# Optimization experiments

Hardware: AMD Instinct MI355X
Metric: run time of the kernel (lower is better)

Reference implementation:

```python
import jax, jax.numpy as jnp
import numpy as np

D_MODEL = 1024
N_HEADS = 16
D_HEAD = D_MODEL // N_HEADS


def setup_inputs() -> dict:
    key = jax.random.key(0)
    ks = jax.random.split(key, 16)
    B, S, D = 2, 2048, D_MODEL
    s = 1.0 / np.sqrt(D)
    inp = {
        "query": jax.random.normal(ks[0], (B, S, D), jnp.float32),
        "key": jax.random.normal(ks[1], (B, S, D), jnp.float32),
        "value": jax.random.normal(ks[2], (B, S, D), jnp.float32),
        "pos_embedding": jax.random.normal(ks[3], (B, S, D), jnp.float32),
        "Wq": jax.random.normal(ks[4], (D, D), jnp.float32) * s,
        "bq": jnp.zeros((D,), jnp.float32),
        "Wk": jax.random.normal(ks[5], (D, D), jnp.float32) * s,
        "bk": jnp.zeros((D,), jnp.float32),
        "Wv": jax.random.normal(ks[6], (D, D), jnp.float32) * s,
        "bv": jnp.zeros((D,), jnp.float32),
        "Wpos": jax.random.normal(ks[7], (D, D), jnp.float32) * s,
        "u_bias": jax.random.normal(ks[8], (N_HEADS, D_HEAD), jnp.float32) * s,
        "v_bias": jax.random.normal(ks[9], (N_HEADS, D_HEAD), jnp.float32) * s,
        "Wout": jax.random.normal(ks[10], (D, D), jnp.float32) * s,
        "bout": jnp.zeros((D,), jnp.float32),
    }
    return inp


def _rel_shift(pos_score):
    # Transformer-XL relative shift: pad one zero column, reshape, drop first row.
    B, H, S1, S2 = pos_score.shape
    zeros = jnp.zeros((B, H, S1, 1), pos_score.dtype)
    padded = jnp.concatenate([zeros, pos_score], axis=-1)  # [B,H,S1,S2+1]
    padded = padded.reshape(B, H, S2 + 1, S1)
    return padded[:, :, 1:].reshape(B, H, S1, S2)


def reference(query, key, value, pos_embedding, Wq, bq, Wk, bk, Wv, bv, Wpos, u_bias, v_bias, Wout, bout):
    B, S, D = query.shape
    H, dh = N_HEADS, D_HEAD
    q = (query @ Wq + bq).reshape(B, S, H, dh)            # [B,S,H,dh]
    k = (key @ Wk + bk).reshape(B, S, H, dh)              # [B,S,H,dh]
    v = (value @ Wv + bv).reshape(B, S, H, dh)            # [B,S,H,dh]
    p = (pos_embedding @ Wpos).reshape(B, S, H, dh)       # [B,S,H,dh]

    content_score = jnp.einsum('bqhd,bkhd->bhqk', q + u_bias, k)
    pos_score = jnp.einsum('bqhd,bkhd->bhqk', q + v_bias, p)
    pos_score = _rel_shift(pos_score)

    score = (content_score + pos_score) / jnp.asarray(np.sqrt(D), score_dtype := content_score.dtype)
    attn = jax.nn.softmax(score, axis=-1)                 # [B,H,S,S]
    context = jnp.einsum('bhqk,bkhd->bqhd', attn, v).reshape(B, S, D)
    out = context @ Wout + bout
    return out, attn
```

## Files before the change

### kernel.cpp

```cpp
#include <hip/hip_runtime.h>

#define S_LEN 2048
#define DM    1024
#define NH    16
#define DH    64
#define BATCH 2
#define S2    ((size_t)S_LEN * S_LEN)

typedef _Float16 half_t;
typedef _Float16 f16x8 __attribute__((ext_vector_type(8)));
typedef _Float16 f16x4 __attribute__((ext_vector_type(4)));
typedef float    f32x4 __attribute__((ext_vector_type(4)));

__device__ __forceinline__ void gll16(const void* g, void* l) {
  __builtin_amdgcn_global_load_lds(
      (const __attribute__((address_space(1))) void*)g,
      (__attribute__((address_space(3))) void*)l, 16, 0, 0);
}

__device__ __forceinline__ void stage_gll(half_t* lds, const half_t* src, int stride) {
  const int t = threadIdx.x, w = t >> 6, lane = t & 63;
  const int c1 = lane & 7, r8 = lane >> 3;
#pragma unroll
  for (int it = 0; it < 4; ++it) {
    int r = w * 32 + it * 8 + r8;
    const half_t* g = src + (size_t)r * stride + ((c1 ^ r8) << 3);
    gll16(g, lds + (size_t)w * 2048 + it * 512);
  }
}

__device__ __forceinline__ void mfma_block(const half_t* At, const half_t* Bt,
                                           int w, int lane, f32x4 acc[2][8]) {
  const int grp = lane >> 4, li = lane & 15;
#pragma unroll
  for (int ks = 0; ks < 2; ++ks) {
    const int chunk = ks * 4 + grp;
    f16x8 a[2], b[8];
#pragma unroll
    for (int fr = 0; fr < 2; ++fr) {
      int r = w * 32 + fr * 16 + li;
      a[fr] = *(const f16x8*)&At[(size_t)(r * 8 + (chunk ^ (r & 7))) * 8];
    }
#pragma unroll
    for (int fc = 0; fc < 8; ++fc) {
      int r = fc * 16 + li;
      b[fc] = *(const f16x8*)&Bt[(size_t)(r * 8 + (chunk ^ (r & 7))) * 8];
    }
#pragma unroll
    for (int fr = 0; fr < 2; ++fr)
#pragma unroll
      for (int fc = 0; fc < 8; ++fc)
        acc[fr][fc] = __builtin_amdgcn_mfma_f32_16x16x32_f16(a[fr], b[fc], acc[fr][fc], 0, 0, 0);
  }
}

template<typename ST>
__device__ __forceinline__ void load8s(const ST* p, float* o) {
  if constexpr (sizeof(ST) == 2) {
    f16x8 v = *(const f16x8*)p;
#pragma unroll
    for (int e = 0; e < 8; ++e) o[e] = (float)v[e];
  } else {
    const float4* q = (const float4*)p;
    float4 a = q[0], b = q[1];
    o[0]=a.x; o[1]=a.y; o[2]=a.z; o[3]=a.w; o[4]=b.x; o[5]=b.y; o[6]=b.z; o[7]=b.w;
  }
}

struct PArgs {
  const float* asrc[4]; half_t* adst[4];
  const float* wsrc[5]; half_t* wdst[5];
};

__global__ __launch_bounds__(256) void prep(PArgs pa, half_t* zbuf) {
  __shared__ float T[64][65];
  const int bx = blockIdx.x, t = threadIdx.x;
  if (bx < 8192) {
    if (bx == 0 && t < 8) {
      float4 z = {0.f, 0.f, 0.f, 0.f};
      ((float4*)zbuf)[t] = z;
    }
    const int mat = bx >> 11, blk = bx & 2047;
    const float* s = pa.asrc[mat];
    half_t* d = pa.adst[mat];
    size_t i = ((size_t)blk * 256 + t) * 8;
    float4 v0 = *(const float4*)(s + i), v1 = *(const float4*)(s + i + 4);
    f16x8 h;
    h[0]=(half_t)v0.x; h[1]=(half_t)v0.y; h[2]=(half_t)v0.z; h[3]=(half_t)v0.w;
    h[4]=(half_t)v1.x; h[5]=(half_t)v1.y; h[6]=(half_t)v1.z; h[7]=(half_t)v1.w;
    *(f16x8*)(d + i) = h;
  } else {
    const int idx = bx - 8192;
    const int z = idx >> 8, rem = idx & 255;
    const int k0 = (rem & 15) * 64, n0 = (rem >> 4) * 64;
    const float* W = pa.wsrc[z];
    half_t* D = pa.wdst[z];
#pragma unroll
    for (int it = 0; it < 4; ++it) {
      int id2 = t + it * 256; int r = id2 >> 4, c4 = (id2 & 15) * 4;
      float4 v = *(const float4*)(W + (size_t)(k0 + r) * DM + n0 + c4);
      T[r][c4] = v.x; T[r][c4 + 1] = v.y; T[r][c4 + 2] = v.z; T[r][c4 + 3] = v.w;
    }
    __syncthreads();
#pragma unroll
    for (int it = 0; it < 2; ++it) {
      int id2 = t + it * 256; int n = id2 >> 3, kc = (id2 & 7) * 8;
      f16x8 o;
#pragma unroll
      for (int e = 0; e < 8; ++e) o[e] = (half_t)T[kc + e][n];
      *(f16x8*)&D[(size_t)(n0 + n) * DM + k0 + kc] = o;
    }
  }
}

struct GArgs {
  const half_t* A[4];  const half_t* Bt[4];
  const float* ba[4]; const float* bu[4]; const float* bv[4];
  half_t* oa[4]; half_t* ob[4]; float* of[4];
};

template<bool F32OUT>
__global__ __launch_bounds__(256) void gemm_k(GArgs g, int K) {
  __shared__ __align__(16) half_t At[128 * 64];
  __shared__ __align__(16) half_t Bt[128 * 64];
  const int z = blockIdx.z;
  const half_t* A = g.A[z];
  const half_t* B = g.Bt[z];
  const int n0 = blockIdx.x * 128, m0 = blockIdx.y * 128;
  const int t = threadIdx.x, w = t >> 6, lane = t & 63;
  const f32x4 zf = {0.f, 0.f, 0.f, 0.f};
  f32x4 acc[2][8];
#pragma unroll
  for (int i = 0; i < 2; ++i)
#pragma unroll
    for (int j = 0; j < 8; ++j) acc[i][j] = zf;

  for (int k0 = 0; k0 < K; k0 += 64) {
    stage_gll(At, A + (size_t)m0 * K + k0, K);
    stage_gll(Bt, B + (size_t)n0 * K + k0, K);
    __syncthreads();
    mfma_block(At, Bt, w, lane, acc);
    __syncthreads();
  }
  const int grp = lane >> 4, li = lane & 15;
#pragma unroll
  for (int fr = 0; fr < 2; ++fr)
#pragma unroll
    for (int fc = 0; fc < 8; ++fc)
#pragma unroll
      for (int r = 0; r < 4; ++r) {
        int row = m0 + w * 32 + fr * 16 + grp * 4 + r;
        int col = n0 + fc * 16 + li;
        float v = acc[fr][fc][r];
        if (g.ba[z]) v += g.ba[z][col];
        if constexpr (F32OUT) {
          g.of[z][(size_t)row * DM + col] = v;
        } else {
          float v1 = v + (g.bu[z] ? g.bu[z][col] : 0.f);
          g.oa[z][(size_t)row * DM + col] = (half_t)v1;
          if (g.ob[z]) g.ob[z][(size_t)row * DM + col] = (half_t)(v + g.bv[z][col]);
        }
      }
}

__global__ __launch_bounds__(256) void vtrans(const half_t* vp, half_t* vT) {
  __shared__ half_t T[64][72];
  const int s0 = blockIdx.x * 64, h = blockIdx.y, b = blockIdx.z;
  const int t = threadIdx.x;
#pragma unroll
  for (int it = 0; it < 2; ++it) {
    int idx = t + it * 256; int s = idx >> 3, c = idx & 7;
    uint4 v = *(const uint4*)(vp + ((size_t)(b * S_LEN + s0 + s)) * DM + h * DH + c * 8);
    *(uint4*)&T[s][c * 8] = v;
  }
  __syncthreads();
  half_t* dst = vT + ((size_t)(b * NH + h)) * DH * S_LEN;
#pragma unroll
  for (int it = 0; it < 2; ++it) {
    int idx = t + it * 256; int d = idx >> 3, sc = (idx & 7) * 8;
    f16x8 o;
#pragma unroll
    for (int e = 0; e < 8; ++e) o[e] = T[sc + e][d];
    *(f16x8*)&dst[(size_t)d * S_LEN + s0 + sc] = o;
  }
}

template<typename ST>
__global__ __launch_bounds__(512, 4) void score_fused(
    const half_t* __restrict__ qu_, const half_t* __restrict__ qv_,
    const half_t* __restrict__ kp_, const half_t* __restrict__ pp_,
    const half_t* __restrict__ zbuf, ST* __restrict__ sc, float* __restrict__ part)
{
  __shared__ __align__(16) half_t RegA[32768];
  __shared__ __align__(16) half_t QV[128 * 64];
  half_t* QU = RegA;
  half_t* Kt = RegA + 8192;
  half_t* Pb = RegA + 16384;
  half_t* Mf = RegA;

  const int bh = blockIdx.z, b = bh >> 4, h = bh & 15;
  const int kt = blockIdx.x, qt = blockIdx.y;
  const int i0 = qt * 128, k0 = kt * 128;
  const int base = 1920 + k0 - i0;
  const int t = threadIdx.x, w = t >> 6, lane = t & 63;
  const int grp = lane >> 4, li = lane & 15;

  {
    const half_t* srcA = qu_ + ((size_t)(b * S_LEN + i0)) * DM + h * DH;
    const half_t* srcB = kp_ + ((size_t)(b * S_LEN + k0)) * DM + h * DH;
    const half_t* srcQ = qv_ + ((size_t)(b * S_LEN + i0)) * DM + h * DH;
#pragma unroll
    for (int p = 0; p < 2; ++p) {
      int cidx = t + p * 512; int r = cidx >> 3, c = cidx & 7;
      size_t off = (size_t)r * DM + ((c ^ (r & 7)) << 3);
      gll16(srcA + off, QU + (size_t)cidx * 8);
      gll16(srcB + off, Kt + (size_t)cidx * 8);
      gll16(srcQ + off, QV + (size_t)cidx * 8);
    }
  }
#pragma unroll
  for (int p = 0; p < 4; ++p) {
    int cidx = t + p * 512; int e = cidx >> 3, c = cidx & 7;
    int jv = base + e; if (jv >= S_LEN + 1) jv -= (S_LEN + 1);
    const half_t* src = (jv == S_LEN)
        ? (zbuf + ((c ^ (e & 7)) << 3))
        : (pp_ + ((size_t)(b * S_LEN + jv)) * DM + h * DH + ((c ^ (e & 7)) << 3));
    gll16(src, Pb + (size_t)cidx * 8);
  }

  f16x8 aq[2];
  {
    int r128 = i0 + 128; if (r128 > S_LEN - 1) r128 = S_LEN - 1;
    const half_t* q128p = qv_ + ((size_t)(b * S_LEN + r128)) * DM + h * DH;
    aq[0] = *(const f16x8*)(q128p + (0 * 4 + grp) * 8);
    aq[1] = *(const f16x8*)(q128p + (1 * 4 + grp) * 8);
  }
  __syncthreads();

  const f32x4 zf = {0.f, 0.f, 0.f, 0.f};
  f32x4 acc_c[8];
#pragma unroll
  for (int j = 0; j < 8; ++j) acc_c[j] = zf;
#pragma unroll
  for (int kk = 0; kk < 2; ++kk) {
    const int chunk = kk * 4 + grp;
    int ra = w * 16 + li;
    f16x8 a = *(const f16x8*)&QU[(size_t)(ra * 8 + (chunk ^ (ra & 7))) * 8];
#pragma unroll
    for (int fc = 0; fc < 8; ++fc) {
      int rb = fc * 16 + li;
      f16x8 bf = *(const f16x8*)&Kt[(size_t)(rb * 8 + (chunk ^ (rb & 7))) * 8];
      acc_c[fc] = __builtin_amdgcn_mfma_f32_16x16x32_f16(a, bf, acc_c[fc], 0, 0, 0);
    }
  }
  f16x8 bm[2][2];
#pragma unroll
  for (int kk = 0; kk < 2; ++kk)
#pragma unroll
    for (int eci = 0; eci < 2; ++eci) {
      int rb = (w + eci * 8) * 16 + li;
      bm[kk][eci] = *(const f16x8*)&Pb[(size_t)(rb * 8 + ((kk * 4 + grp) ^ (rb & 7))) * 8];
    }
  __syncthreads();

  for (int rf = 0; rf < 8; ++rf) {
    f32x4 am[2] = {zf, zf};
#pragma unroll
    for (int kk = 0; kk < 2; ++kk) {
      int ra = rf * 16 + li;
      f16x8 a = *(const f16x8*)&QV[(size_t)(ra * 8 + ((kk * 4 + grp) ^ (ra & 7))) * 8];
#pragma unroll
      for (int eci = 0; eci < 2; ++eci)
        am[eci] = __builtin_amdgcn_mfma_f32_16x16x32_f16(a, bm[kk][eci], am[eci], 0, 0, 0);
    }
#pragma unroll
    for (int eci = 0; eci < 2; ++eci) {
      int ec = w + eci * 8;
      if (!(ec == 15 && li == 15)) {
        f16x4 hv;
#pragma unroll
        for (int r = 0; r < 4; ++r) hv[r] = (half_t)am[eci][r];
        *(f16x4*)&Mf[(size_t)(((ec * 8 + rf) * 4 + grp) * 64 + li * 4)] = hv;
      }
    }
  }

  {
    f32x4 am0 = zf;
#pragma unroll
    for (int kk = 0; kk < 2; ++kk)
      am0 = __builtin_amdgcn_mfma_f32_16x16x32_f16(aq[kk], bm[kk][0], am0, 0, 0, 0);
    if (grp == 0) {
      int e = w * 16 + li;
      Mf[(size_t)(((120 + (e >> 4)) * 4 + ((e >> 2) & 3)) * 64 + 60 + (e & 3))] = (half_t)am0[0];
    }
  }
  __syncthreads();

  ST* sb = sc + (size_t)bh * S2;
  float lsum[4] = {0.f, 0.f, 0.f, 0.f};
#pragma unroll
  for (int fc = 0; fc < 8; ++fc) {
#pragma unroll
    for (int rr = 0; rr < 4; ++rr) {
      int q = w * 16 + grp * 4 + rr;
      int k = fc * 16 + li;
      int e = k - q + 127;
      int jv = base + e;
      int dlt = (jv >= S_LEN + 1) ? 1 : 0;
      int rM = q + dlt;
      float mval;
      if (rM < 128) {
        int ec = e >> 4, ei = e & 15, rf = rM >> 4, ri = rM & 15;
        mval = (float)Mf[(size_t)(((ec * 8 + rf) * 4 + (ri >> 2)) * 64 + ei * 4 + (ri & 3))];
      } else {
        mval = (float)Mf[(size_t)(((120 + (e >> 4)) * 4 + ((e >> 2) & 3)) * 64 + 60 + (e & 3))];
      }
      float s = (acc_c[fc][rr] + mval) * 0.03125f;
      float ev = __expf(s);
      sb[(size_t)(i0 + q) * S_LEN + k0 + k] = (ST)ev;
      lsum[rr] += ev;
    }
  }
#pragma unroll
  for (int rr = 0; rr < 4; ++rr) {
    float v = lsum[rr];
#pragma unroll
    for (int d = 1; d < 16; d <<= 1) v += __shfl_xor(v, d);
    if (li == 0)
      part[((size_t)bh * S_LEN + i0 + w * 16 + grp * 4 + rr) * 16 + kt] = v;
  }
}

template<typename ST>
__global__ __launch_bounds__(256) void av_attn(const ST* sc, const half_t* vT, const float* part,
                                               float* attn, half_t* ctx) {
  __shared__ __align__(16) half_t Vt[2][64 * 128];
  __shared__ float Ls[128];
  const int bh = blockIdx.y, b = bh >> 4, h = bh & 15;
  const int q0 = blockIdx.x * 128;
  const int t = threadIdx.x;
  if (t < 128) {
    const float* pp = part + ((size_t)bh * S_LEN + q0 + t) * 16;
    float L = 0.f;
#pragma unroll
    for (int k = 0; k < 16; ++k) L += pp[k];
    Ls[t] = 1.f / L;
  }
  const ST* sb = sc + (size_t)bh * S2;
  float* ab = attn + (size_t)bh * S2;
  const half_t* vb = vT + (size_t)bh * (DH * S_LEN);
  const int w = t >> 6, lane = t & 63, grp = lane >> 4, li = lane & 15;
  const int c1 = lane & 15, d4 = lane >> 4;
  const f32x4 zf = {0.f, 0.f, 0.f, 0.f};
  f32x4 acc[2][4];
#pragma unroll
  for (int i = 0; i < 2; ++i)
#pragma unroll
    for (int j = 0; j < 4; ++j) acc[i][j] = zf;

#pragma unroll
  for (int it = 0; it < 4; ++it) {
    int d = w * 16 + it * 4 + d4;
    gll16(vb + (size_t)d * S_LEN + ((c1 ^ (d & 15)) << 3), Vt[0] + (size_t)w * 2048 + it * 512);
  }
  __syncthreads();
  int cur = 0;

  for (int kt = 0; kt < 16; ++kt) {
    if (kt + 1 < 16) {
#pragma unroll
      for (int it = 0; it < 4; ++it) {
        int d = w * 16 + it * 4 + d4;
        gll16(vb + (size_t)d * S_LEN + (kt + 1) * 128 + ((c1 ^ (d & 15)) << 3),
              Vt[cur ^ 1] + (size_t)w * 2048 + it * 512);
      }
    }
#pragma unroll
    for (int ks = 0; ks < 4; ++ks) {
      f16x8 pa[2];
#pragma unroll
      for (int fr = 0; fr < 2; ++fr) {
        int r128 = w * 32 + fr * 16 + li;
        int row = q0 + r128;
        int col = kt * 128 + ks * 32 + grp * 8;
        float sv[8];
        load8s(&sb[(size_t)row * S_LEN + col], sv);
        float rL = Ls[r128];
#pragma unroll
        for (int e = 0; e < 8; ++e) sv[e] *= rL;
        float4* dst = (float4*)&ab[(size_t)row * S_LEN + col];
        float4 w0 = {sv[0], sv[1], sv[2], sv[3]};
        float4 w1 = {sv[4], sv[5], sv[6], sv[7]};
        dst[0] = w0; dst[1] = w1;
        f16x8 ph;
#pragma unroll
        for (int e = 0; e < 8; ++e) ph[e] = (half_t)sv[e];
        pa[fr] = ph;
      }
      f16x8 bf[4];
#pragma unroll
      for (int fc = 0; fc < 4; ++fc) {
        int d = fc * 16 + li; int chunk = ks * 4 + grp;
        bf[fc] = *(const f16x8*)&Vt[cur][(size_t)(d * 16 + (chunk ^ (d & 15))) * 8];
      }
#pragma unroll
      for (int fr = 0; fr < 2; ++fr)
#pragma unroll
        for (int fc = 0; fc < 4; ++fc)
          acc[fr][fc] = __builtin_amdgcn_mfma_f32_16x16x32_f16(pa[fr], bf[fc], acc[fr][fc], 0, 0, 0);
    }
    __syncthreads();
    cur ^= 1;
  }
#pragma unroll
  for (int fr = 0; fr < 2; ++fr)
#pragma unroll
    for (int fc = 0; fc < 4; ++fc)
#pragma unroll
      for (int r = 0; r < 4; ++r) {
        int q = q0 + w * 32 + fr * 16 + grp * 4 + r;
        int d = fc * 16 + li;
        ctx[((size_t)(b * S_LEN + q)) * DM + h * DH + d] = (half_t)acc[fr][fc][r];
      }
}

extern "C" void kernel_launch(void* const* d_in, const int* in_sizes, int n_in,
                              void* d_out, int out_size, void* d_ws, size_t ws_size,
                              hipStream_t stream) {
  (void)in_sizes; (void)n_in; (void)out_size;

  const float* query  = (const float*)d_in[0];
  const float* key    = (const float*)d_in[1];
  const float* value  = (const float*)d_in[2];
  const float* pos    = (const float*)d_in[3];
  const float* Wq     = (const float*)d_in[4];
  const float* bq     = (const float*)d_in[5];
  const float* Wk     = (const float*)d_in[6];
  const float* bk     = (const float*)d_in[7];
  const float* Wv     = (const float*)d_in[8];
  const float* bv     = (const float*)d_in[9];
  const float* Wpos   = (const float*)d_in[10];
  const float* u_bias = (const float*)d_in[11];
  const float* v_bias = (const float*)d_in[12];
  const float* Wout   = (const float*)d_in[13];
  const float* bout   = (const float*)d_in[14];

  float* out  = (float*)d_out;
  float* attn = out + (size_t)BATCH * S_LEN * DM;

  char* ws = (char*)d_ws;
  half_t* Wt   = (half_t*)(ws);
  half_t* Af16 = (half_t*)(ws + 10485760);
  float*  part = (float*)(ws + 10485760);
  half_t* qu   = (half_t*)(ws + 44040192);
  half_t* qv   = (half_t*)(ws + 52428800);
  half_t* kp   = (half_t*)(ws + 60817408);
  half_t* pp   = (half_t*)(ws + 69206016);
  half_t* vp   = (half_t*)(ws + 77594624);
  half_t* vT   = (half_t*)(ws + 85983232);
  half_t* ctx  = (half_t*)(ws + 77594624);
  half_t* zbuf = (half_t*)(ws + 94371840);
  half_t* scH  = (half_t*)(ws + 94375936);
  const bool fast = ws_size >= (size_t)94375936 + (size_t)BATCH * NH * S2 * 2;

  dim3 blk(256);

  PArgs pa;
  pa.asrc[0] = query; pa.asrc[1] = key; pa.asrc[2] = value; pa.asrc[3] = pos;
  for (int i = 0; i < 4; ++i) pa.adst[i] = Af16 + (size_t)i * BATCH * S_LEN * DM;
  pa.wsrc[0] = Wq; pa.wsrc[1] = Wk; pa.wsrc[2] = Wv; pa.wsrc[3] = Wpos; pa.wsrc[4] = Wout;
  for (int i = 0; i < 5; ++i) pa.wdst[i] = Wt + (size_t)i * DM * DM;
  prep<<<dim3(8192 + 1280), blk, 0, stream>>>(pa, zbuf);

  GArgs ga{};
  for (int i = 0; i < 4; ++i) {
    ga.A[i]  = Af16 + (size_t)i * BATCH * S_LEN * DM;
    ga.Bt[i] = Wt + (size_t)i * DM * DM;
  }
  ga.ba[0] = bq; ga.ba[1] = bk; ga.ba[2] = bv; ga.ba[3] = nullptr;
  ga.bu[0] = u_bias; ga.bv[0] = v_bias;
  ga.oa[0] = qu; ga.oa[1] = kp; ga.oa[2] = vp; ga.oa[3] = pp;
  ga.ob[0] = qv;
  gemm_k<false><<<dim3(8, 32, 4), blk, 0, stream>>>(ga, DM);

  vtrans<<<dim3(32, 16, 2), blk, 0, stream>>>(vp, vT);

  dim3 g_sc(16, 16, 32);
  dim3 blk5(512);
  if (fast) {
    score_fused<half_t><<<g_sc, blk5, 0, stream>>>(qu, qv, kp, pp, zbuf, scH, part);
    av_attn<half_t><<<dim3(16, 32), blk, 0, stream>>>(scH, vT, part, attn, ctx);
  } else {
    float* scF = attn;
    score_fused<float><<<g_sc, blk5, 0, stream>>>(qu, qv, kp, pp, zbuf, scF, part);
    av_attn<float><<<dim3(16, 32), blk, 0, stream>>>(scF, vT, part, attn, ctx);
  }

  GArgs go{};
  go.A[0] = ctx; go.Bt[0] = Wt + (size_t)4 * DM * DM;
  go.ba[0] = bout; go.of[0] = out;
  gemm_k<true><<<dim3(8, 32, 1), blk, 0, stream>>>(go, DM);
}
```

Before: 548.7 us.

## Split AV attention over key dimension into two partial passes and combine

The attention-times-V kernel now runs over a third grid dimension that splits the 16 key tiles into two halves. Each half writes a partial fp16 context into its own workspace buffer, and a new combine2 kernel sums them into the final context. The original grid of 512 blocks was small relative to the GPU's CU count, so the split is meant to raise occupancy and parallelism. In exchange it adds an extra launch, extra context traffic, and an fp16 rounding of each partial sum before the add.

```diff
diff --git a/kernel.cpp b/kernel.cpp
--- a/kernel.cpp
+++ b/kernel.cpp
@@ -6,6 +6,7 @@
 #define DH    64
 #define BATCH 2
 #define S2    ((size_t)S_LEN * S_LEN)
+#define CTXSZ ((size_t)BATCH * S_LEN * DM)
 
 typedef _Float16 half_t;
 typedef _Float16 f16x8 __attribute__((ext_vector_type(8)));
@@ -334,11 +335,12 @@
 
 template<typename ST>
 __global__ __launch_bounds__(256) void av_attn(const ST* sc, const half_t* vT, const float* part,
-                                               float* attn, half_t* ctx) {
+                                               float* attn, half_t* ctxp) {
   __shared__ __align__(16) half_t Vt[2][64 * 128];
   __shared__ float Ls[128];
   const int bh = blockIdx.y, b = bh >> 4, h = bh & 15;
   const int q0 = blockIdx.x * 128;
+  const int kz = blockIdx.z;
   const int t = threadIdx.x;
   if (t < 128) {
     const float* pp = part + ((size_t)bh * S_LEN + q0 + t) * 16;
@@ -350,8 +352,10 @@
   const ST* sb = sc + (size_t)bh * S2;
   float* ab = attn + (size_t)bh * S2;
   const half_t* vb = vT + (size_t)bh * (DH * S_LEN);
+  half_t* ctx = ctxp + (size_t)kz * CTXSZ;
   const int w = t >> 6, lane = t & 63, grp = lane >> 4, li = lane & 15;
   const int c1 = lane & 15, d4 = lane >> 4;
+  const int kt0 = kz * 8, kt1 = kt0 + 8;
   const f32x4 zf = {0.f, 0.f, 0.f, 0.f};
   f32x4 acc[2][4];
 #pragma unroll
@@ -362,13 +366,14 @@
 #pragma unroll
   for (int it = 0; it < 4; ++it) {
     int d = w * 16 + it * 4 + d4;
-    gll16(vb + (size_t)d * S_LEN + ((c1 ^ (d & 15)) << 3), Vt[0] + (size_t)w * 2048 + it * 512);
+    gll16(vb + (size_t)d * S_LEN + kt0 * 128 + ((c1 ^ (d & 15)) << 3),
+          Vt[0] + (size_t)w * 2048 + it * 512);
   }
   __syncthreads();
   int cur = 0;
 
-  for (int kt = 0; kt < 16; ++kt) {
-    if (kt + 1 < 16) {
+  for (int kt = kt0; kt < kt1; ++kt) {
+    if (kt + 1 < kt1) {
 #pragma unroll
       for (int it = 0; it < 4; ++it) {
         int d = w * 16 + it * 4 + d4;
@@ -423,6 +428,16 @@
         int d = fc * 16 + li;
         ctx[((size_t)(b * S_LEN + q)) * DM + h * DH + d] = (half_t)acc[fr][fc][r];
       }
+}
+
+__global__ __launch_bounds__(256) void combine2(const half_t* a, const half_t* b, half_t* o) {
+  size_t i = ((size_t)blockIdx.x * 256 + threadIdx.x) * 8;
+  f16x8 va = *(const f16x8*)(a + i);
+  f16x8 vb = *(const f16x8*)(b + i);
+  f16x8 vo;
+#pragma unroll
+  for (int e = 0; e < 8; ++e) vo[e] = (half_t)((float)va[e] + (float)vb[e]);
+  *(f16x8*)(o + i) = vo;
 }
 
 extern "C" void kernel_launch(void* const* d_in, const int* in_sizes, int n_in,
@@ -453,6 +468,7 @@
   half_t* Wt   = (half_t*)(ws);
   half_t* Af16 = (half_t*)(ws + 10485760);
   float*  part = (float*)(ws + 10485760);
+  half_t* ctxp = (half_t*)(ws + 14680064);
   half_t* qu   = (half_t*)(ws + 44040192);
   half_t* qv   = (half_t*)(ws + 52428800);
   half_t* kp   = (half_t*)(ws + 60817408);
@@ -468,14 +484,14 @@
 
   PArgs pa;
   pa.asrc[0] = query; pa.asrc[1] = key; pa.asrc[2] = value; pa.asrc[3] = pos;
-  for (int i = 0; i < 4; ++i) pa.adst[i] = Af16 + (size_t)i * BATCH * S_LEN * DM;
+  for (int i = 0; i < 4; ++i) pa.adst[i] = Af16 + (size_t)i * CTXSZ;
   pa.wsrc[0] = Wq; pa.wsrc[1] = Wk; pa.wsrc[2] = Wv; pa.wsrc[3] = Wpos; pa.wsrc[4] = Wout;
   for (int i = 0; i < 5; ++i) pa.wdst[i] = Wt + (size_t)i * DM * DM;
   prep<<<dim3(8192 + 1280), blk, 0, stream>>>(pa, zbuf);
 
   GArgs ga{};
   for (int i = 0; i < 4; ++i) {
-    ga.A[i]  = Af16 + (size_t)i * BATCH * S_LEN * DM;
+    ga.A[i]  = Af16 + (size_t)i * CTXSZ;
     ga.Bt[i] = Wt + (size_t)i * DM * DM;
   }
   ga.ba[0] = bq; ga.ba[1] = bk; ga.ba[2] = bv; ga.ba[3] = nullptr;
@@ -490,12 +506,13 @@
   dim3 blk5(512);
   if (fast) {
     score_fused<half_t><<<g_sc, blk5, 0, stream>>>(qu, qv, kp, pp, zbuf, scH, part);
-    av_attn<half_t><<<dim3(16, 32), blk, 0, stream>>>(scH, vT, part, attn, ctx);
+    av_attn<half_t><<<dim3(16, 32, 2), blk, 0, stream>>>(scH, vT, part, attn, ctxp);
   } else {
     float* scF = attn;
     score_fused<float><<<g_sc, blk5, 0, stream>>>(qu, qv, kp, pp, zbuf, scF, part);
-    av_attn<float><<<dim3(16, 32), blk, 0, stream>>>(scF, vT, part, attn, ctx);
-  }
+    av_attn<float><<<dim3(16, 32, 2), blk, 0, stream>>>(scF, vT, part, attn, ctxp);
+  }
+  combine2<<<dim3((int)(CTXSZ / 8 / 256)), blk, 0, stream>>>(ctxp, ctxp + CTXSZ, ctx);
 
   GArgs go{};
   go.A[0] = ctx; go.Bt[0] = Wt + (size_t)4 * DM * DM;
```

Result: no change. 548.1 us (-0.1%).

## Shrink score kernel LDS by loading pos rows directly and storing shifted matrix

Applied to the files above, without the earlier changes.

The score kernel no longer stages the 256-row positional block in shared memory. Each thread loads its two positional B-fragments straight from global memory into registers. The positional scores are scattered during the MFMA epilogue into a pre-shifted 128x132 matrix, so the softmax loop reads them with a plain index instead of recomputing the relative shift. This cuts shared memory per block from about 80 KB to about 50 KB and raises the launch-bounds occupancy hint from 4 to 6. In exchange it adds uncoalesced global fragment loads and scattered 2-byte LDS stores that may hit bank conflicts.

```diff
diff --git a/kernel.cpp b/kernel.cpp
--- a/kernel.cpp
+++ b/kernel.cpp
@@ -6,10 +6,10 @@
 #define DH    64
 #define BATCH 2
 #define S2    ((size_t)S_LEN * S_LEN)
+#define CTXSZ ((size_t)BATCH * S_LEN * DM)
 
 typedef _Float16 half_t;
 typedef _Float16 f16x8 __attribute__((ext_vector_type(8)));
-typedef _Float16 f16x4 __attribute__((ext_vector_type(4)));
 typedef float    f32x4 __attribute__((ext_vector_type(4)));
 
 __device__ __forceinline__ void gll16(const void* g, void* l) {
@@ -186,17 +186,16 @@
 }
 
 template<typename ST>
-__global__ __launch_bounds__(512, 4) void score_fused(
+__global__ __launch_bounds__(512, 6) void score_fused(
     const half_t* __restrict__ qu_, const half_t* __restrict__ qv_,
     const half_t* __restrict__ kp_, const half_t* __restrict__ pp_,
     const half_t* __restrict__ zbuf, ST* __restrict__ sc, float* __restrict__ part)
 {
-  __shared__ __align__(16) half_t RegA[32768];
+  __shared__ __align__(16) half_t MsR[16896];
   __shared__ __align__(16) half_t QV[128 * 64];
-  half_t* QU = RegA;
-  half_t* Kt = RegA + 8192;
-  half_t* Pb = RegA + 16384;
-  half_t* Mf = RegA;
+  half_t* QU = MsR;
+  half_t* Kt = MsR + 8192;
+  half_t* Ms = MsR;
 
   const int bh = blockIdx.z, b = bh >> 4, h = bh & 15;
   const int kt = blockIdx.x, qt = blockIdx.y;
@@ -218,22 +217,20 @@
       gll16(srcQ + off, QV + (size_t)cidx * 8);
     }
   }
-#pragma unroll
-  for (int p = 0; p < 4; ++p) {
-    int cidx = t + p * 512; int e = cidx >> 3, c = cidx & 7;
-    int jv = base + e; if (jv >= S_LEN + 1) jv -= (S_LEN + 1);
-    const half_t* src = (jv == S_LEN)
-        ? (zbuf + ((c ^ (e & 7)) << 3))
-        : (pp_ + ((size_t)(b * S_LEN + jv)) * DM + h * DH + ((c ^ (e & 7)) << 3));
-    gll16(src, Pb + (size_t)cidx * 8);
-  }
-
-  f16x8 aq[2];
-  {
-    int r128 = i0 + 128; if (r128 > S_LEN - 1) r128 = S_LEN - 1;
-    const half_t* q128p = qv_ + ((size_t)(b * S_LEN + r128)) * DM + h * DH;
-    aq[0] = *(const f16x8*)(q128p + (0 * 4 + grp) * 8);
-    aq[1] = *(const f16x8*)(q128p + (1 * 4 + grp) * 8);
+
+  const int e0 = w * 16 + li, e1 = (w + 8) * 16 + li;
+  const int dlt0 = (base + e0 >= S_LEN + 1) ? 1 : 0;
+  const int dlt1 = (base + e1 >= S_LEN + 1) ? 1 : 0;
+  f16x8 bm[2][2];
+#pragma unroll
+  for (int eci = 0; eci < 2; ++eci) {
+    int e_row = eci ? e1 : e0;
+    int jv = base + e_row; if (jv >= S_LEN + 1) jv -= (S_LEN + 1);
+    const half_t* srcp = (jv == S_LEN) ? zbuf
+        : pp_ + ((size_t)(b * S_LEN + jv)) * DM + h * DH;
+#pragma unroll
+    for (int kk = 0; kk < 2; ++kk)
+      bm[kk][eci] = *(const f16x8*)(srcp + (kk * 4 + grp) * 8);
   }
   __syncthreads();
 
@@ -253,14 +250,6 @@
       acc_c[fc] = __builtin_amdgcn_mfma_f32_16x16x32_f16(a, bf, acc_c[fc], 0, 0, 0);
     }
   }
-  f16x8 bm[2][2];
-#pragma unroll
-  for (int kk = 0; kk < 2; ++kk)
-#pragma unroll
-    for (int eci = 0; eci < 2; ++eci) {
-      int rb = (w + eci * 8) * 16 + li;
-      bm[kk][eci] = *(const f16x8*)&Pb[(size_t)(rb * 8 + ((kk * 4 + grp) ^ (rb & 7))) * 8];
-    }
   __syncthreads();
 
   for (int rf = 0; rf < 8; ++rf) {
@@ -269,31 +258,37 @@
     for (int kk = 0; kk < 2; ++kk) {
       int ra = rf * 16 + li;
       f16x8 a = *(const f16x8*)&QV[(size_t)(ra * 8 + ((kk * 4 + grp) ^ (ra & 7))) * 8];
-#pragma unroll
-      for (int eci = 0; eci < 2; ++eci)
-        am[eci] = __builtin_amdgcn_mfma_f32_16x16x32_f16(a, bm[kk][eci], am[eci], 0, 0, 0);
+      am[0] = __builtin_amdgcn_mfma_f32_16x16x32_f16(a, bm[kk][0], am[0], 0, 0, 0);
+      am[1] = __builtin_amdgcn_mfma_f32_16x16x32_f16(a, bm[kk][1], am[1], 0, 0, 0);
     }
 #pragma unroll
     for (int eci = 0; eci < 2; ++eci) {
-      int ec = w + eci * 8;
-      if (!(ec == 15 && li == 15)) {
-        f16x4 hv;
-#pragma unroll
-        for (int r = 0; r < 4; ++r) hv[r] = (half_t)am[eci][r];
-        *(f16x4*)&Mf[(size_t)(((ec * 8 + rf) * 4 + grp) * 64 + li * 4)] = hv;
+      int e = eci ? e1 : e0;
+      int dlt = eci ? dlt1 : dlt0;
+#pragma unroll
+      for (int r = 0; r < 4; ++r) {
+        int rM = rf * 16 + grp * 4 + r;
+        int q = rM - dlt;
+        int k = e + q - 127;
+        if ((unsigned)q < 128u && (unsigned)k < 128u)
+          Ms[q * 132 + k] = (half_t)am[eci][r];
       }
     }
   }
 
   {
+    f16x8 aq0, aq1;
+    {
+      int r128 = i0 + 128; if (r128 > S_LEN - 1) r128 = S_LEN - 1;
+      const half_t* q128p = qv_ + ((size_t)(b * S_LEN + r128)) * DM + h * DH;
+      aq0 = *(const f16x8*)(q128p + (0 * 4 + grp) * 8);
+      aq1 = *(const f16x8*)(q128p + (1 * 4 + grp) * 8);
+    }
     f32x4 am0 = zf;
-#pragma unroll
-    for (int kk = 0; kk < 2; ++kk)
-      am0 = __builtin_amdgcn_mfma_f32_16x16x32_f16(aq[kk], bm[kk][0], am0, 0, 0, 0);
-    if (grp == 0) {
-      int e = w * 16 + li;
-      Mf[(size_t)(((120 + (e >> 4)) * 4 + ((e >> 2) & 3)) * 64 + 60 + (e & 3))] = (half_t)am0[0];
-    }
+    am0 = __builtin_amdgcn_mfma_f32_16x16x32_f16(aq0, bm[0][0], am0, 0, 0, 0);
+    am0 = __builtin_amdgcn_mfma_f32_16x16x32_f16(aq1, bm[1][0], am0, 0, 0, 0);
+    if (grp == 0 && dlt0 == 1)
+      Ms[127 * 132 + e0] = (half_t)am0[0];
   }
   __syncthreads();
 
@@ -305,17 +300,7 @@
     for (int rr = 0; rr < 4; ++rr) {
       int q = w * 16 + grp * 4 + rr;
       int k = fc * 16 + li;
-      int e = k - q + 127;
-      int jv = base + e;
-      int dlt = (jv >= S_LEN + 1) ? 1 : 0;
-      int rM = q + dlt;
-      float mval;
-      if (rM < 128) {
-        int ec = e >> 4, ei = e & 15, rf = rM >> 4, ri = rM & 15;
-        mval = (float)Mf[(size_t)(((ec * 8 + rf) * 4 + (ri >> 2)) * 64 + ei * 4 + (ri & 3))];
-      } else {
-        mval = (float)Mf[(size_t)(((120 + (e >> 4)) * 4 + ((e >> 2) & 3)) * 64 + 60 + (e & 3))];
-      }
+      float mval = (float)Ms[q * 132 + k];
       float s = (acc_c[fc][rr] + mval) * 0.03125f;
       float ev = __expf(s);
       sb[(size_t)(i0 + q) * S_LEN + k0 + k] = (ST)ev;
@@ -468,14 +453,14 @@
 
   PArgs pa;
   pa.asrc[0] = query; pa.asrc[1] = key; pa.asrc[2] = value; pa.asrc[3] = pos;
-  for (int i = 0; i < 4; ++i) pa.adst[i] = Af16 + (size_t)i * BATCH * S_LEN * DM;
+  for (int i = 0; i < 4; ++i) pa.adst[i] = Af16 + (size_t)i * CTXSZ;
   pa.wsrc[0] = Wq; pa.wsrc[1] = Wk; pa.wsrc[2] = Wv; pa.wsrc[3] = Wpos; pa.wsrc[4] = Wout;
   for (int i = 0; i < 5; ++i) pa.wdst[i] = Wt + (size_t)i * DM * DM;
   prep<<<dim3(8192 + 1280), blk, 0, stream>>>(pa, zbuf);
 
   GArgs ga{};
   for (int i = 0; i < 4; ++i) {
-    ga.A[i]  = Af16 + (size_t)i * BATCH * S_LEN * DM;
+    ga.A[i]  = Af16 + (size_t)i * CTXSZ;
     ga.Bt[i] = Wt + (size_t)i * DM * DM;
   }
   ga.ba[0] = bq; ga.ba[1] = bk; ga.ba[2] = bv; ga.ba[3] = nullptr;
```

New measurement: 511.7 us. 1.07x faster.
